# Optimization experiments

Hardware: AMD Instinct MI355X
Metric: run time of the kernel (lower is better)

The kernel has to match this reference:

```python
import jax, jax.numpy as jnp
import numpy as np
from jax.scipy.special import logsumexp

B = 64          # batch
SIZE = 256      # lattice width -> SIZE+1 states
LEN_PAT = 32    # pattern length
NEG = -1e9      # finite stand-in for -inf (exp underflows to 0 exactly in fp32)


def setup_inputs() -> dict:
    key = jax.random.key(0)
    k1, k2, k3, k4 = jax.random.split(key, 4)
    logits = jax.random.normal(k1, (B, 3, SIZE), dtype=jnp.float32)
    Q = jax.random.normal(k2, (1, 3, SIZE + 1, SIZE + 1), dtype=jnp.float32) * 0.1
    pattern = jax.random.randint(k3, (LEN_PAT,), 0, 3, dtype=jnp.int32)
    ls = jax.random.randint(k4, (B,), 0, SIZE, dtype=jnp.int32)
    return {"logits": logits, "Q": Q, "pattern": pattern, "ls": ls}


def build_P(logits):
    # Faithful vectorization of P_: P[b,ch,i,j] = sum_{k=i}^{j-1} log y[b,ch,k] if j>i,
    # -inf for j<=i (rows 0..SIZE-1), and row SIZE is all zeros (never masked in the loop).
    C = jax.nn.log_softmax(logits, axis=1)                              # [B,3,SIZE]
    cs = jnp.concatenate([jnp.zeros_like(C[..., :1]), jnp.cumsum(C, -1)], -1)  # [B,3,SIZE+1]
    diff = cs[:, :, None, :] - cs[:, :, :, None]                        # cs[j]-cs[i]
    idx = jnp.arange(SIZE + 1)
    upper = idx[None, :] > idx[:, None]                                 # j > i
    P = jnp.where(upper, diff, NEG)                                     # [B,3,S+1,S+1]
    P = P.at[:, :, SIZE, :].set(0.0)
    return P


def sum_alpha(P, Q, pattern):
    bs, s1 = P.shape[0], P.shape[-1]
    a0 = jnp.full((bs, s1), NEG, dtype=P.dtype).at[:, 0].set(0.0)
    n0 = jnp.zeros((bs,), dtype=P.dtype)  # logsumexp(a0) == 0

    def step(carry, c):
        la, ln = carry
        T = P[:, c] + Q[0, c]                       # [B,S+1,S+1]
        a = logsumexp(T + la[:, :, None], axis=1)   # reduce over source state
        n = ln + logsumexp(a, axis=-1)
        a = a + (ln - n)[:, None]                   # online renormalization
        return (a, n), a + n[:, None]

    _, outs = jax.lax.scan(step, (a0, n0), pattern)            # [LEN,B,S+1]
    return jnp.concatenate([a0[:, None, :], jnp.transpose(outs, (1, 0, 2))], axis=1)


def sum_beta(P, Q, pattern, ls):
    bs, s1 = P.shape[0], P.shape[-1]
    b0 = jnp.full((bs, s1), NEG, dtype=P.dtype).at[jnp.arange(bs), ls].set(0.0)
    n0 = jnp.zeros((bs,), dtype=P.dtype)

    def step(carry, c):
        lb, ln = carry
        T = P[:, c] + Q[0, c]
        b = logsumexp(T + lb[:, None, :], axis=2)   # reduce over target state
        n = ln + logsumexp(b, axis=-1)
        b = b + (ln - n)[:, None]
        return (b, n), b + n[:, None]

    _, outs = jax.lax.scan(step, (b0, n0), pattern[::-1])      # positions LEN-1..0
    outs = jnp.flip(jnp.transpose(outs, (1, 0, 2)), axis=1)    # positions 0..LEN-1
    return jnp.concatenate([outs, b0[:, None, :]], axis=1)


def reference(logits, Q, pattern, ls):
    bs = logits.shape[0]
    P = build_P(logits)                                         # [B,3,S+1,S+1]
    a = sum_alpha(P, Q, pattern)                                # [B,LEN+1,S+1]
    b = sum_beta(P, Q, pattern, ls)                             # [B,LEN+1,S+1]
    ll = a + b
    M = a[jnp.arange(bs), -1, ls]                               # [B]
    p = a + b - M[:, None, None]                                # single marginals
    Tpat = P[:, pattern] + Q[0][pattern]                        # [B,LEN,S+1,S+1]
    t = a[:, :-1, :, None] + b[:, 1:, None, :] + Tpat - M[:, None, None, None]
    return (M, ll, a, b, ls, p, t)
```

## Files before the change

kernel.cpp:

```cpp
#include <hip/hip_runtime.h>

#define NEGV (-1e9f)

constexpr int BN   = 64;
constexpr int S1   = 257;
constexpr int LEN  = 32;
constexpr int CH   = S1 * S1;
constexpr int ROWS = LEN + 1;
constexpr int ABSZ = BN * ROWS * S1;
constexpr int EQP  = 260;
constexpr int EQC  = S1 * EQP;

constexpr int OFF_M  = 0;
constexpr int OFF_LL = 64;
constexpr int OFF_A  = OFF_LL + ABSZ;
constexpr int OFF_B  = OFF_A + ABSZ;
constexpr int OFF_LS = OFF_B + ABSZ;
constexpr int OFF_P  = OFF_LS + 64;
constexpr int OFF_T  = OFF_P + ABSZ;

constexpr int WS_CS  = 0;
constexpr int WS_M   = 64 * 771;
constexpr int WS_SCR = WS_M + 64;

constexpr int SC_CSD = 0;
constexpr int SC_EQ  = 2 * 64 * 771;
constexpr int SC_EQT = SC_EQ + 3 * EQC;
constexpr int SC_END = SC_EQT + 3 * EQC;

__device__ __forceinline__ double dexp(double x) {
  double t = x * 1.4426950408889634;
  double n = floor(t);
  float  f = (float)(t - n);
  double r = (double)exp2f(f);
  long long bb = __double_as_longlong(r);
  bb += ((long long)n) << 52;
  return __longlong_as_double(bb);
}
__device__ __forceinline__ float dlogf(double x) {
  if (!(x > 1e-300)) return NEGV;
  long long bb = __double_as_longlong(x);
  int e = (int)((bb >> 52) & 0x7ff) - 1023;
  bb = (bb & 0xFFFFFFFFFFFFFLL) | 0x3FF0000000000000LL;
  float m = (float)__longlong_as_double(bb);
  return __logf(m) + (float)e * 0.69314718055994531f;
}

__device__ __forceinline__ void barL() {
  asm volatile("s_waitcnt lgkmcnt(0)" ::: "memory");
  __builtin_amdgcn_s_barrier();
  __builtin_amdgcn_sched_barrier(0);
}

__global__ __launch_bounds__(256) void k_pre(const float* __restrict__ logits,
                                             const float* __restrict__ Q,
                                             const int* __restrict__ ls,
                                             float* __restrict__ ws,
                                             float* __restrict__ scr,
                                             float* __restrict__ out) {
  const int blk = blockIdx.x;
  const int tid = threadIdx.x;
  if (blk < 3 * S1) {
    const int c = blk / S1, i = blk - c * S1;
    float* EQ = scr + SC_EQ;
    const float* Qr = Q + c * CH + i * S1;
    for (int j = tid; j < S1; j += 256) {
      float e = __expf(Qr[j]);
      EQ[c * EQC + i * EQP + j] = ((i < j) || (i == 256)) ? e : 0.f;
    }
    return;
  }
  if (blk < 3 * S1 + 51) {
    const int g = blk - 3 * S1;
    const int c = g / 17, grp = g - c * 17;
    const int i = grp * 16 + (tid & 15);
    float* EQT = scr + SC_EQT;
    if (i < S1) {
      const float* Qci = Q + c * CH + i * S1;
      for (int j = tid >> 4; j < S1; j += 16) {
        float e = __expf(Qci[j]);
        EQT[c * EQC + j * EQP + i] = ((j > i) || (j == 256)) ? e : 0.f;
      }
    }
    return;
  }
  const int b = blk - 3 * S1 - 51;
  __shared__ float sC[3][256];
  {
    float l0 = logits[(b*3+0)*256 + tid];
    float l1 = logits[(b*3+1)*256 + tid];
    float l2 = logits[(b*3+2)*256 + tid];
    float mm = fmaxf(l0, fmaxf(l1, l2));
    float lse = mm + __logf(__expf(l0-mm) + __expf(l1-mm) + __expf(l2-mm));
    sC[0][tid] = l0 - lse;
    sC[1][tid] = l1 - lse;
    sC[2][tid] = l2 - lse;
  }
  __syncthreads();
  const int w = tid >> 6, lane = tid & 63;
  double* csD = (double*)(scr + SC_CSD);
  if (w < 3) {
    float*  cs32 = ws + WS_CS + b*771 + w*257;
    double* csd  = csD + b*771 + w*257;
    if (lane == 0) { cs32[0] = 0.f; csd[0] = 0.0; }
    double carry = 0.0;
    for (int t = 0; t < 4; ++t) {
      double v = (double)sC[w][t*64 + lane];
      #pragma unroll
      for (int off = 1; off < 64; off <<= 1) {
        double o = __shfl_up(v, off);
        if (lane >= off) v += o;
      }
      double r = carry + v;
      cs32[t*64 + lane + 1] = (float)r;
      csd [t*64 + lane + 1] = r;
      carry += __shfl(v, 63);
    }
  }
  if (tid == 0) out[OFF_LS + b] = (float)ls[b];
}

__global__ __launch_bounds__(512, 2) void k_rec(const float* __restrict__ scr,
                                                const int* __restrict__ pattern,
                                                const int* __restrict__ ls,
                                                float* __restrict__ ws,
                                                float* __restrict__ out) {
  __shared__ double ecsP[3][257], ecsM[3][257];
  __shared__ double wDp[2][258];
  __shared__ double AD[258];
  __shared__ double part[8][260];
  __shared__ float eqR[3][257];
  __shared__ float eqC[3][257];
  __shared__ int patS[LEN];
  const int tid = threadIdx.x;
  const bool isBeta = (blockIdx.x >= BN);
  const int b = isBeta ? (blockIdx.x - BN) : blockIdx.x;
  const float* EQ  = scr + SC_EQ;
  const float* EQT = scr + SC_EQT;
  const double* csD = (const double*)(scr + SC_CSD) + b * 771;

  if (tid < LEN) patS[tid] = pattern[tid];
  const int lsb = ls[b];
  for (int idx = tid; idx < 771; idx += 512) {
    int c = idx / 257, j = idx - c * 257;
    double x = csD[idx];
    ecsP[c][j] = dexp(x);
    ecsM[c][j] = dexp(-x);
    eqR[c][j] = EQ[c * EQC + 256 * EQP + j];
    eqC[c][j] = EQ[c * EQC + j * EQP + 256];
  }
  float* outab = out + (isBeta ? OFF_B : OFF_A) + b * (ROWS * S1);
  const int w = tid >> 6, l = tid & 63;
  const int k0 = w << 5, col0 = l << 2;
  const bool act = isBeta ? (col0 < k0 + 31) : (k0 < col0 + 3);

  if (tid < S1) {
    if (!isBeta) {
      __builtin_nontemporal_store((tid == 0) ? 0.f : NEGV, &outab[tid]);
    } else {
      AD[tid] = (tid == lsb) ? 1.0 : 0.0;
      __builtin_nontemporal_store((tid == lsb) ? 0.f : NEGV, &outab[LEN * S1 + tid]);
    }
  }
  __syncthreads();
  if (tid < S1) {
    if (!isBeta) wDp[0][tid] = (tid == 0) ? 1.0 : 0.0;
    else         wDp[0][tid] = (tid == lsb) ? ecsP[patS[LEN-1]][tid] : 0.0;
  }
  float4 tile[32];
  {
    const float* bp = (isBeta ? EQT : EQ) +
                      (isBeta ? patS[LEN-1] : patS[0]) * EQC + k0 * EQP + col0;
    if (act) {
      #pragma unroll
      for (int kk = 0; kk < 32; ++kk) tile[kk] = *(const float4*)(bp + kk * EQP);
    }
  }
  barL();

  int cur = 0;
  if (!isBeta) {
    for (int step = 0; step < LEN; ++step, cur ^= 1) {
      const int c = patS[step];
      const double* wc = wDp[cur];
      double a0 = 0, a1 = 0, a2 = 0, a3 = 0;
      if (act) {
        #pragma unroll
        for (int kk = 0; kk < 32; ++kk) {
          float4 e = tile[kk];
          double wv = wc[k0 + kk];
          a0 += wv * (double)e.x;
          a1 += wv * (double)e.y;
          a2 += wv * (double)e.z;
          a3 += wv * (double)e.w;
        }
        if (step + 1 < LEN) {
          const float* bp = EQ + patS[step+1] * EQC + k0 * EQP + col0;
          #pragma unroll
          for (int kk = 0; kk < 32; ++kk) tile[kk] = *(const float4*)(bp + kk * EQP);
        }
      }
      part[w][col0] = a0; part[w][col0+1] = a1;
      part[w][col0+2] = a2; part[w][col0+3] = a3;
      double c2 = 0;
      if (l < 32) c2 = wc[k0 + l] * (double)eqC[c][k0 + l];
      c2 += __shfl_xor(c2, 1); c2 += __shfl_xor(c2, 2);
      c2 += __shfl_xor(c2, 4); c2 += __shfl_xor(c2, 8); c2 += __shfl_xor(c2, 16);
      if (l == 0) part[w][256] = c2;
      barL();
      if (tid < S1) {
        const int j = tid;
        const double wA256 = wDp[cur][256];
        double sum = ((part[0][j] + part[1][j]) + (part[2][j] + part[3][j]))
                   + ((part[4][j] + part[5][j]) + (part[6][j] + part[7][j]));
        double Ar = ecsP[c][j] * sum + wA256 * (double)eqR[c][j];
        float lo = dlogf(Ar);
        __builtin_nontemporal_store(lo, &outab[(step + 1) * S1 + j]);
        if (step == LEN - 1) {
          if (j == lsb) { out[OFF_M + b] = lo; ws[WS_M + b] = lo; }
        } else {
          wDp[cur ^ 1][j] = (j < 256) ? Ar * ecsM[patS[step+1]][j] : Ar;
        }
      }
      barL();
    }
  } else {
    for (int ss = 0; ss < LEN; ++ss, cur ^= 1) {
      const int step = LEN - 1 - ss;
      const int c = patS[step];
      const double* wc = wDp[cur];
      double a0 = 0, a1 = 0, a2 = 0, a3 = 0;
      if (act) {
        #pragma unroll
        for (int kk = 0; kk < 32; ++kk) {
          float4 e = tile[kk];
          double wv = wc[k0 + kk];
          a0 += wv * (double)e.x;
          a1 += wv * (double)e.y;
          a2 += wv * (double)e.z;
          a3 += wv * (double)e.w;
        }
        if (ss + 1 < LEN) {
          const float* bp = EQT + patS[step-1] * EQC + k0 * EQP + col0;
          #pragma unroll
          for (int kk = 0; kk < 32; ++kk) tile[kk] = *(const float4*)(bp + kk * EQP);
        }
      }
      part[w][col0] = a0; part[w][col0+1] = a1;
      part[w][col0+2] = a2; part[w][col0+3] = a3;
      double r2 = 0;
      if (l < 32) r2 = AD[k0 + l] * (double)eqR[c][k0 + l];
      r2 += __shfl_xor(r2, 1); r2 += __shfl_xor(r2, 2);
      r2 += __shfl_xor(r2, 4); r2 += __shfl_xor(r2, 8); r2 += __shfl_xor(r2, 16);
      if (l == 0) part[w][256] = r2;
      barL();
      if (tid < S1) {
        const int i = tid;
        const double wB256 = wDp[cur][256];
        double sum = ((part[0][i] + part[1][i]) + (part[2][i] + part[3][i]))
                   + ((part[4][i] + part[5][i]) + (part[6][i] + part[7][i]));
        double Ar;
        if (i < 256) Ar = ecsM[c][i] * (sum + (double)eqC[c][i] * wB256);
        else         Ar = sum + (double)eqR[c][256] * AD[256];
        __builtin_nontemporal_store(dlogf(Ar), &outab[step * S1 + i]);
        AD[i] = Ar;
        if (ss < LEN - 1) wDp[cur ^ 1][i] = Ar * ecsP[patS[step-1]][i];
      }
      barL();
    }
  }
}

__global__ __launch_bounds__(256) void k_t(const float* __restrict__ Q,
                                           const int* __restrict__ pattern,
                                           const float* __restrict__ ws,
                                           float* __restrict__ out) {
  __shared__ float r1[257], r2[257], c1[257], c2[257];
  const int bk = blockIdx.x;
  const int b = bk >> 5, k = bk & 31;
  const int c = pattern[k];
  const float Mb = ws[WS_M + b];
  const int tid = threadIdx.x;
  const float* cs  = ws + WS_CS + b*771 + c*257;
  const float* ar  = out + OFF_A + (b*ROWS + k) * S1;
  const float* br  = out + OFF_B + (b*ROWS + k + 1) * S1;
  const float* br0 = out + OFF_B + (b*ROWS + k) * S1;
  for (int i = tid; i < S1; i += 256) {
    float av = ar[i], cv = cs[i], bv = br[i];
    r1[i] = av - cv - Mb;
    r2[i] = av - Mb + ((i == 256) ? 0.f : NEGV);
    c1[i] = bv + cv;
    c2[i] = bv;
    float ll = av + br0[i];
    out[OFF_LL + (b*ROWS + k) * S1 + i] = ll;
    out[OFF_P  + (b*ROWS + k) * S1 + i] = ll - Mb;
    if (k == 0) {
      float l2 = out[OFF_A + (b*ROWS + LEN) * S1 + i] +
                 out[OFF_B + (b*ROWS + LEN) * S1 + i];
      out[OFF_LL + (b*ROWS + LEN) * S1 + i] = l2;
      out[OFF_P  + (b*ROWS + LEN) * S1 + i] = l2 - Mb;
    }
  }
  __syncthreads();
  const float* Qc = Q + c*CH;
  float* tb = out + OFF_T + (size_t)bk * CH;
  const int lead = (4 - (bk & 3)) & 3;
  const int main4 = (CH - lead) >> 2;
  const int tail = CH - lead - (main4 << 2);
  if (tid < lead) {
    int j = tid;
    float v = (j > 0) ? (r1[0] + c1[j]) : (r2[0] + c2[0]);
    tb[j] = Qc[j] + v;
  }
  if (tid >= 8 && tid < 8 + tail) {
    int idx = lead + (main4 << 2) + (tid - 8);
    int i = idx / 257, j = idx - i * 257;
    float v = (j > i) ? (r1[i] + c1[j]) : (r2[i] + c2[j]);
    tb[idx] = Qc[idx] + v;
  }
  for (int v4 = tid; v4 < main4; v4 += 256) {
    const int base = lead + (v4 << 2);
    const float* qp = Qc + base;
    int i0 = base / 257, j0 = base - i0 * 257;
    float4 o;
    {
      int j = j0,     i = i0; if (j >= 257) { j -= 257; ++i; }
      o.x = qp[0] + ((j > i) ? (r1[i] + c1[j]) : (r2[i] + c2[j]));
    }
    {
      int j = j0 + 1, i = i0; if (j >= 257) { j -= 257; ++i; }
      o.y = qp[1] + ((j > i) ? (r1[i] + c1[j]) : (r2[i] + c2[j]));
    }
    {
      int j = j0 + 2, i = i0; if (j >= 257) { j -= 257; ++i; }
      o.z = qp[2] + ((j > i) ? (r1[i] + c1[j]) : (r2[i] + c2[j]));
    }
    {
      int j = j0 + 3, i = i0; if (j >= 257) { j -= 257; ++i; }
      o.w = qp[3] + ((j > i) ? (r1[i] + c1[j]) : (r2[i] + c2[j]));
    }
    *(float4*)(tb + base) = o;
  }
}

extern "C" void kernel_launch(void* const* d_in, const int* in_sizes, int n_in,
                              void* d_out, int out_size, void* d_ws, size_t ws_size,
                              hipStream_t stream) {
  const float* logits = (const float*)d_in[0];
  const float* Q      = (const float*)d_in[1];
  const int* pattern  = (const int*)d_in[2];
  const int* ls       = (const int*)d_in[3];
  float* out = (float*)d_out;
  float* ws  = (float*)d_ws;

  const size_t need = (size_t)(WS_SCR + SC_END) * sizeof(float);
  float* scr = (ws_size >= need) ? (ws + WS_SCR) : (out + OFF_T);

  k_pre<<<3*S1 + 51 + BN, 256, 0, stream>>>(logits, Q, ls, ws, scr, out);
  k_rec<<<2*BN, 512, 0, stream>>>(scr, pattern, ls, ws, out);
  k_t<<<BN*LEN, 256, 0, stream>>>(Q, pattern, ws, out);
}
```

Baseline: 327.8 us.

## Compact active triangular tiles onto threads and use nontemporal stores for T output

The recurrence kernel now assigns threads only to the active triangular tiles, packed contiguously, and zeroes the partial-sum buffer once instead of writing zero partials from idle threads. One otherwise idle wave handles the column-256 correction reduction over all 256 entries. In the final T-output kernel, plain stores become nontemporal stores, including the float4 vector path, to avoid cache pollution on the large write stream. The aim is to cut per-step wasted work and LDS writes in the latency-bound recurrence and to ease write traffic in the output stage.

New measurement: 351.2 us. 7.1% more time.

```diff
diff --git a/kernel.cpp b/kernel.cpp
--- a/kernel.cpp
+++ b/kernel.cpp
@@ -1,6 +1,8 @@
 #include <hip/hip_runtime.h>
 
 #define NEGV (-1e9f)
+
+typedef float vf4 __attribute__((ext_vector_type(4)));
 
 constexpr int BN   = 64;
 constexpr int S1   = 257;
@@ -149,10 +151,28 @@
     eqR[c][j] = EQ[c * EQC + 256 * EQP + j];
     eqC[c][j] = EQ[c * EQC + j * EQP + 256];
   }
+  {
+    double* pf = &part[0][0];
+    for (int idx = tid; idx < 8 * 260; idx += 512) pf[idx] = 0.0;
+  }
+  int rr = 0, cc = 0;
+  bool act = false;
+  {
+    int base = 0;
+    #pragma unroll
+    for (int r = 0; r < 8; ++r) {
+      int v = isBeta ? 8 * (r + 1) : (64 - 8 * r);
+      if (tid >= base && tid < base + v) {
+        rr = r;
+        cc = isBeta ? (tid - base) : (8 * r + (tid - base));
+        act = true;
+      }
+      base += v;
+    }
+  }
   float* outab = out + (isBeta ? OFF_B : OFF_A) + b * (ROWS * S1);
   const int w = tid >> 6, l = tid & 63;
-  const int k0 = w << 5, col0 = l << 2;
-  const bool act = isBeta ? (col0 < k0 + 31) : (k0 < col0 + 3);
+  const int k0 = rr << 5, col0 = cc << 2;
 
   if (tid < S1) {
     if (!isBeta) {
@@ -168,13 +188,11 @@
     else         wDp[0][tid] = (tid == lsb) ? ecsP[patS[LEN-1]][tid] : 0.0;
   }
   float4 tile[32];
-  {
+  if (act) {
     const float* bp = (isBeta ? EQT : EQ) +
                       (isBeta ? patS[LEN-1] : patS[0]) * EQC + k0 * EQP + col0;
-    if (act) {
-      #pragma unroll
-      for (int kk = 0; kk < 32; ++kk) tile[kk] = *(const float4*)(bp + kk * EQP);
-    }
+    #pragma unroll
+    for (int kk = 0; kk < 32; ++kk) tile[kk] = *(const float4*)(bp + kk * EQP);
   }
   barL();
 
@@ -183,8 +201,8 @@
     for (int step = 0; step < LEN; ++step, cur ^= 1) {
       const int c = patS[step];
       const double* wc = wDp[cur];
-      double a0 = 0, a1 = 0, a2 = 0, a3 = 0;
       if (act) {
+        double a0 = 0, a1 = 0, a2 = 0, a3 = 0;
         #pragma unroll
         for (int kk = 0; kk < 32; ++kk) {
           float4 e = tile[kk];
@@ -199,14 +217,18 @@
           #pragma unroll
           for (int kk = 0; kk < 32; ++kk) tile[kk] = *(const float4*)(bp + kk * EQP);
         }
-      }
-      part[w][col0] = a0; part[w][col0+1] = a1;
-      part[w][col0+2] = a2; part[w][col0+3] = a3;
-      double c2 = 0;
-      if (l < 32) c2 = wc[k0 + l] * (double)eqC[c][k0 + l];
-      c2 += __shfl_xor(c2, 1); c2 += __shfl_xor(c2, 2);
-      c2 += __shfl_xor(c2, 4); c2 += __shfl_xor(c2, 8); c2 += __shfl_xor(c2, 16);
-      if (l == 0) part[w][256] = c2;
+        part[rr][col0] = a0; part[rr][col0+1] = a1;
+        part[rr][col0+2] = a2; part[rr][col0+3] = a3;
+      } else if (w == 5) {
+        double c2 = wc[l]       * (double)eqC[c][l]
+                  + wc[l + 64]  * (double)eqC[c][l + 64]
+                  + wc[l + 128] * (double)eqC[c][l + 128]
+                  + wc[l + 192] * (double)eqC[c][l + 192];
+        c2 += __shfl_xor(c2, 1);  c2 += __shfl_xor(c2, 2);
+        c2 += __shfl_xor(c2, 4);  c2 += __shfl_xor(c2, 8);
+        c2 += __shfl_xor(c2, 16); c2 += __shfl_xor(c2, 32);
+        if (l == 0) part[0][256] = c2;
+      }
       barL();
       if (tid < S1) {
         const int j = tid;
@@ -229,8 +251,8 @@
       const int step = LEN - 1 - ss;
       const int c = patS[step];
       const double* wc = wDp[cur];
-      double a0 = 0, a1 = 0, a2 = 0, a3 = 0;
       if (act) {
+        double a0 = 0, a1 = 0, a2 = 0, a3 = 0;
         #pragma unroll
         for (int kk = 0; kk < 32; ++kk) {
           float4 e = tile[kk];
@@ -245,14 +267,18 @@
           #pragma unroll
           for (int kk = 0; kk < 32; ++kk) tile[kk] = *(const float4*)(bp + kk * EQP);
         }
-      }
-      part[w][col0] = a0; part[w][col0+1] = a1;
-      part[w][col0+2] = a2; part[w][col0+3] = a3;
-      double r2 = 0;
-      if (l < 32) r2 = AD[k0 + l] * (double)eqR[c][k0 + l];
-      r2 += __shfl_xor(r2, 1); r2 += __shfl_xor(r2, 2);
-      r2 += __shfl_xor(r2, 4); r2 += __shfl_xor(r2, 8); r2 += __shfl_xor(r2, 16);
-      if (l == 0) part[w][256] = r2;
+        part[rr][col0] = a0; part[rr][col0+1] = a1;
+        part[rr][col0+2] = a2; part[rr][col0+3] = a3;
+      } else if (w == 5) {
+        double r2 = AD[l]       * (double)eqR[c][l]
+                  + AD[l + 64]  * (double)eqR[c][l + 64]
+                  + AD[l + 128] * (double)eqR[c][l + 128]
+                  + AD[l + 192] * (double)eqR[c][l + 192];
+        r2 += __shfl_xor(r2, 1);  r2 += __shfl_xor(r2, 2);
+        r2 += __shfl_xor(r2, 4);  r2 += __shfl_xor(r2, 8);
+        r2 += __shfl_xor(r2, 16); r2 += __shfl_xor(r2, 32);
+        if (l == 0) part[0][256] = r2;
+      }
       barL();
       if (tid < S1) {
         const int i = tid;
@@ -310,19 +336,19 @@
   if (tid < lead) {
     int j = tid;
     float v = (j > 0) ? (r1[0] + c1[j]) : (r2[0] + c2[0]);
-    tb[j] = Qc[j] + v;
+    __builtin_nontemporal_store(Qc[j] + v, tb + j);
   }
   if (tid >= 8 && tid < 8 + tail) {
     int idx = lead + (main4 << 2) + (tid - 8);
     int i = idx / 257, j = idx - i * 257;
     float v = (j > i) ? (r1[i] + c1[j]) : (r2[i] + c2[j]);
-    tb[idx] = Qc[idx] + v;
+    __builtin_nontemporal_store(Qc[idx] + v, tb + idx);
   }
   for (int v4 = tid; v4 < main4; v4 += 256) {
     const int base = lead + (v4 << 2);
     const float* qp = Qc + base;
     int i0 = base / 257, j0 = base - i0 * 257;
-    float4 o;
+    vf4 o;
     {
       int j = j0,     i = i0; if (j >= 257) { j -= 257; ++i; }
       o.x = qp[0] + ((j > i) ? (r1[i] + c1[j]) : (r2[i] + c2[j]));
@@ -339,7 +365,7 @@
       int j = j0 + 3, i = i0; if (j >= 257) { j -= 257; ++i; }
       o.w = qp[3] + ((j > i) ? (r1[i] + c1[j]) : (r2[i] + c2[j]));
     }
-    *(float4*)(tb + base) = o;
+    __builtin_nontemporal_store(o, (vf4*)(tb + base));
   }
 }
 
```

## Tile T output by row slabs with Q slab cached in LDS, split ll/p kernel

Applied to the files above, without the earlier changes.

The k_t kernel is restructured so each block owns a 32-row slab of one channel's Q matrix, loads it once into shared memory, and reuses it across 32 (batch, position) pairs that use that channel, instead of re-reading the full Q matrix from global memory per (b,k). T stores become nontemporal. The ll/p writes move to a separate elementwise kernel. This cuts Q read traffic but adds a kernel launch, a serial pattern scan, and per-pair syncs. It also assumes the 2*count slot mapping covers exactly 64 slots.

Result: faster. 293.1 us (-10.6%).

```diff
diff --git a/kernel.cpp b/kernel.cpp
--- a/kernel.cpp
+++ b/kernel.cpp
@@ -271,75 +271,82 @@
   }
 }
 
+__global__ __launch_bounds__(256) void k_llp(const float* __restrict__ ws,
+                                             float* __restrict__ out) {
+  int idx = blockIdx.x * 256 + threadIdx.x;
+  if (idx >= ABSZ) return;
+  int b = idx / (ROWS * S1);
+  float a = out[OFF_A + idx];
+  float bb = out[OFF_B + idx];
+  float ll = a + bb;
+  __builtin_nontemporal_store(ll, out + OFF_LL + idx);
+  __builtin_nontemporal_store(ll - ws[WS_M + b], out + OFF_P + idx);
+}
+
 __global__ __launch_bounds__(256) void k_t(const float* __restrict__ Q,
                                            const int* __restrict__ pattern,
                                            const float* __restrict__ ws,
                                            float* __restrict__ out) {
-  __shared__ float r1[257], r2[257], c1[257], c2[257];
-  const int bk = blockIdx.x;
-  const int b = bk >> 5, k = bk & 31;
-  const int c = pattern[k];
-  const float Mb = ws[WS_M + b];
-  const int tid = threadIdx.x;
-  const float* cs  = ws + WS_CS + b*771 + c*257;
-  const float* ar  = out + OFF_A + (b*ROWS + k) * S1;
-  const float* br  = out + OFF_B + (b*ROWS + k + 1) * S1;
-  const float* br0 = out + OFF_B + (b*ROWS + k) * S1;
-  for (int i = tid; i < S1; i += 256) {
-    float av = ar[i], cv = cs[i], bv = br[i];
-    r1[i] = av - cv - Mb;
-    r2[i] = av - Mb + ((i == 256) ? 0.f : NEGV);
-    c1[i] = bv + cv;
-    c2[i] = bv;
-    float ll = av + br0[i];
-    out[OFF_LL + (b*ROWS + k) * S1 + i] = ll;
-    out[OFF_P  + (b*ROWS + k) * S1 + i] = ll - Mb;
-    if (k == 0) {
-      float l2 = out[OFF_A + (b*ROWS + LEN) * S1 + i] +
-                 out[OFF_B + (b*ROWS + LEN) * S1 + i];
-      out[OFF_LL + (b*ROWS + LEN) * S1 + i] = l2;
-      out[OFF_P  + (b*ROWS + LEN) * S1 + i] = l2 - Mb;
-    }
+  __shared__ float qs[32 * 257];
+  __shared__ float c1[257], c2[257], r1[32], r2[32];
+  __shared__ int Kc[3][32];
+  __shared__ int nK[3];
+  const int tid  = threadIdx.x;
+  const int slab = blockIdx.x >> 6;
+  const int slot = blockIdx.x & 63;
+  if (tid == 0) {
+    int n0 = 0, n1 = 0, n2 = 0;
+    for (int k = 0; k < LEN; ++k) {
+      int c = pattern[k];
+      if (c == 0) Kc[0][n0++] = k;
+      else if (c == 1) Kc[1][n1++] = k;
+      else Kc[2][n2++] = k;
+    }
+    nK[0] = n0; nK[1] = n1; nK[2] = n2;
   }
   __syncthreads();
-  const float* Qc = Q + c*CH;
-  float* tb = out + OFF_T + (size_t)bk * CH;
-  const int lead = (4 - (bk & 3)) & 3;
-  const int main4 = (CH - lead) >> 2;
-  const int tail = CH - lead - (main4 << 2);
-  if (tid < lead) {
-    int j = tid;
-    float v = (j > 0) ? (r1[0] + c1[j]) : (r2[0] + c2[0]);
-    tb[j] = Qc[j] + v;
-  }
-  if (tid >= 8 && tid < 8 + tail) {
-    int idx = lead + (main4 << 2) + (tid - 8);
-    int i = idx / 257, j = idx - i * 257;
-    float v = (j > i) ? (r1[i] + c1[j]) : (r2[i] + c2[j]);
-    tb[idx] = Qc[idx] + v;
-  }
-  for (int v4 = tid; v4 < main4; v4 += 256) {
-    const int base = lead + (v4 << 2);
-    const float* qp = Qc + base;
-    int i0 = base / 257, j0 = base - i0 * 257;
-    float4 o;
-    {
-      int j = j0,     i = i0; if (j >= 257) { j -= 257; ++i; }
-      o.x = qp[0] + ((j > i) ? (r1[i] + c1[j]) : (r2[i] + c2[j]));
-    }
-    {
-      int j = j0 + 1, i = i0; if (j >= 257) { j -= 257; ++i; }
-      o.y = qp[1] + ((j > i) ? (r1[i] + c1[j]) : (r2[i] + c2[j]));
-    }
-    {
-      int j = j0 + 2, i = i0; if (j >= 257) { j -= 257; ++i; }
-      o.z = qp[2] + ((j > i) ? (r1[i] + c1[j]) : (r2[i] + c2[j]));
-    }
-    {
-      int j = j0 + 3, i = i0; if (j >= 257) { j -= 257; ++i; }
-      o.w = qp[3] + ((j > i) ? (r1[i] + c1[j]) : (r2[i] + c2[j]));
-    }
-    *(float4*)(tb + base) = o;
+  int c, chunk;
+  {
+    const int s0 = 2 * nK[0], s1 = s0 + 2 * nK[1];
+    if (slot < s0)      { c = 0; chunk = slot; }
+    else if (slot < s1) { c = 1; chunk = slot - s0; }
+    else                { c = 2; chunk = slot - s1; }
+  }
+  const int nk = nK[c];
+  const int i0 = slab << 5;
+  const int R  = (257 - i0 < 32) ? (257 - i0) : 32;
+  for (int idx = tid; idx < R * 257; idx += 256)
+    qs[idx] = Q[c * CH + i0 * 257 + idx];
+  const int p0 = chunk << 5;
+  for (int pp = 0; pp < 32; ++pp) {
+    const int p = p0 + pp;
+    const int b = p / nk, kidx = p - b * nk;
+    const int k = Kc[c][kidx];
+    __syncthreads();
+    const float Mb = ws[WS_M + b];
+    const float* cs = ws + WS_CS + b * 771 + c * 257;
+    const float* ar = out + OFF_A + (b * ROWS + k) * S1;
+    const float* br = out + OFF_B + (b * ROWS + k + 1) * S1;
+    for (int j = tid; j < S1; j += 256) {
+      float bv = br[j], cv = cs[j];
+      c1[j] = bv + cv;
+      c2[j] = bv;
+    }
+    if (tid < R) {
+      const int i = i0 + tid;
+      float av = ar[i];
+      r1[tid] = av - cs[i] - Mb;
+      r2[tid] = av - Mb + ((i == 256) ? 0.f : NEGV);
+    }
+    __syncthreads();
+    float* tb = out + OFF_T + (size_t)((b << 5) + k) * CH + i0 * 257;
+    int ii = 0, j = tid;
+    for (int idx = tid; idx < R * 257; idx += 256) {
+      float v = (j > i0 + ii) ? (r1[ii] + c1[j]) : (r2[ii] + c2[j]);
+      __builtin_nontemporal_store(qs[idx] + v, tb + idx);
+      j += 256;
+      if (j >= 257) { j -= 257; ++ii; }
+    }
   }
 }
 
@@ -358,5 +365,6 @@
 
   k_pre<<<3*S1 + 51 + BN, 256, 0, stream>>>(logits, Q, ls, ws, scr, out);
   k_rec<<<2*BN, 512, 0, stream>>>(scr, pattern, ls, ws, out);
-  k_t<<<BN*LEN, 256, 0, stream>>>(Q, pattern, ws, out);
-}
+  k_llp<<<(ABSZ + 255)/256, 256, 0, stream>>>(ws, out);
+  k_t<<<9 * 64, 256, 0, stream>>>(Q, pattern, ws, out);
+}
```
